# Optimization experiments

Hardware: AMD Instinct MI355X
Metric: run time of the kernel (lower is better)

Reference implementation:

```python
import jax, jax.numpy as jnp
import numpy as np

# Fixed supermask = [3, 4, 16, 28, 0, 0, 0, 3]:
#   preproc: relu(Linear x3); l1 = GCN(x); l2 = GCN(l1); l3 = GCN(l2);
#   out = relu(Linear z3((l1+l2+l3)/3))
HIDDEN = 64


def gcn_conv(h, W, b, src, dst, norm, n_nodes):
    # PyG GCNConv: h' = scatter_add(norm * (hW)[src] -> dst) + b
    hw = h @ W                                  # [N, F]
    msg = hw[src] * norm[:, None]               # gather + scale  [E+N, F]
    agg = jax.ops.segment_sum(msg, dst, num_segments=n_nodes)
    return agg + b


def setup_inputs() -> dict:
    key = jax.random.key(0)
    ks = jax.random.split(key, 12)
    N, E, NFEAT, NCLASS = 100000, 1000000, 256, 40
    x = jax.random.normal(ks[0], (N, NFEAT), dtype=jnp.float32)
    edge_index = jax.random.randint(ks[1], (2, E), 0, N, dtype=jnp.int64)
    s = 1.0 / np.sqrt(NFEAT)
    h = 1.0 / np.sqrt(HIDDEN)
    return {
        "x": x,
        "edge_index": edge_index,
        "Wx": jax.random.uniform(ks[2], (NFEAT, HIDDEN), jnp.float32, -s, s),
        "bx": jnp.zeros((HIDDEN,), jnp.float32),
        "W1": jax.random.uniform(ks[3], (HIDDEN, HIDDEN), jnp.float32, -h, h),
        "b1": jnp.zeros((HIDDEN,), jnp.float32),
        "W2": jax.random.uniform(ks[4], (HIDDEN, HIDDEN), jnp.float32, -h, h),
        "b2": jnp.zeros((HIDDEN,), jnp.float32),
        "W3": jax.random.uniform(ks[5], (HIDDEN, HIDDEN), jnp.float32, -h, h),
        "b3": jnp.zeros((HIDDEN,), jnp.float32),
        "Wz": jax.random.uniform(ks[6], (HIDDEN, NCLASS), jnp.float32, -h, h),
        "bz": jnp.zeros((NCLASS,), jnp.float32),
    }


def reference(x, edge_index, Wx, bx, W1, b1, W2, b2, W3, b3, Wz, bz):
    n = x.shape[0]
    # add self-loops (PyG GCNConv default)
    loop = jnp.arange(n, dtype=edge_index.dtype)
    src = jnp.concatenate([edge_index[0], loop])
    dst = jnp.concatenate([edge_index[1], loop])
    deg = jax.ops.segment_sum(jnp.ones_like(dst, dtype=x.dtype), dst, num_segments=n)
    dinv = jnp.where(deg > 0, jax.lax.rsqrt(deg), 0.0)
    norm = dinv[src] * dinv[dst]                 # [E+N]

    h0 = jax.nn.relu(x @ Wx + bx)                # x_3(relu) o x3(Linear)
    l1 = gcn_conv(h0, W1, b1, src, dst, norm, n)
    l2 = gcn_conv(l1, W2, b2, src, dst, norm, n)
    l3 = gcn_conv(l2, W3, b3, src, dst, norm, n)
    z = (l1 + l2 + l3) / 3.0
    return jax.nn.relu(z @ Wz + bz)
```

## Files before the change

### kernel.cpp

```cpp
#include <hip/hip_runtime.h>

#define NFEAT 256
#define HID 64
#define NCLASS 40
#define EPB 2048
#define BCAP 8192

typedef _Float16 half8 __attribute__((ext_vector_type(8)));
typedef float floatx4 __attribute__((ext_vector_type(4)));

__device__ __forceinline__ int wave_iscan(int v, int lane) {
    #pragma unroll
    for (int o = 1; o < 64; o <<= 1) {
        int u = __shfl_up(v, o, 64);
        if (lane >= o) v += u;
    }
    return v;
}

template<int NT>
__device__ __forceinline__ int block_iscan(int v, int t, int* wsum) {
    const int NW = NT / 64;
    int lane = t & 63, wv = t >> 6;
    int s = wave_iscan(v, lane);
    if (lane == 63) wsum[wv] = s;
    __syncthreads();
    if (wv == 0) {
        int w = (lane < NW) ? wsum[lane] : 0;
        #pragma unroll
        for (int o = 1; o < NW; o <<= 1) {
            int u = __shfl_up(w, o, 64);
            if (lane >= o) w += u;
        }
        if (lane < NW) wsum[lane] = w;
    }
    __syncthreads();
    int add = (wv > 0) ? wsum[wv - 1] : 0;
    return s + add;
}

struct BinSM {
    int lcnt[256], loff[256], lcur[256], gbase[256], wsum[4];
    int sdst[EPB];
    int words[EPB];
};
#define WT_BYTES (64 * 264 * 2)
#define SMSZ (sizeof(BinSM) > WT_BYTES ? sizeof(BinSM) : WT_BYTES)

__global__ __launch_bounds__(256) void k_pre(const int* __restrict__ src, const int* __restrict__ dst,
                                             int* __restrict__ bcur, int* __restrict__ bwords,
                                             int nbuckets, int E, int nbin,
                                             const float* __restrict__ W1, const float* __restrict__ W2,
                                             const float* __restrict__ W3, _Float16* __restrict__ Wt16,
                                             const float* __restrict__ x, const float* __restrict__ Wx,
                                             const float* __restrict__ bx, _Float16* __restrict__ h0,
                                             int N, int ngemm) {
    __shared__ __align__(16) char smraw[SMSZ];
    int t = threadIdx.x;
    int bid = blockIdx.x;

    if (bid >= nbin && bid < nbin + 3) {
        int l = bid - nbin;
        const float* Ws = (l == 0) ? W1 : (l == 1) ? W2 : W3;
        _Float16* wt = Wt16 + l * 4096;
        for (int i = t; i < 4096; i += 256) {
            int col = i >> 6, k = i & 63;
            wt[i] = (_Float16)Ws[k * HID + col];
        }
        return;
    }

    if (bid >= nbin + 3) {
        _Float16 (*Wt)[264] = (_Float16 (*)[264])smraw;
        {
            int c = t & 63, k0 = (t >> 6) * 64;
            for (int k = k0; k < k0 + 64; ++k)
                Wt[c][k] = (_Float16)Wx[k * HID + c];
        }
        __syncthreads();
        int lane = t & 63, wv = t >> 6;
        int lg = lane >> 4, ln = lane & 15;
        int gb = bid - nbin - 3;
        int wid = gb * 4 + wv;
        int nw = ngemm * 4;
        float bb[4];
        #pragma unroll
        for (int g = 0; g < 4; ++g) bb[g] = bx[g * 16 + ln];
        int ntiles = N >> 4;
        for (int tile = wid; tile < ntiles; tile += nw) {
            int row0 = tile << 4;
            const float* xr = x + (size_t)(row0 + ln) * NFEAT + lg * 8;
            float4 av[16];
            #pragma unroll
            for (int ks = 0; ks < 8; ++ks) {
                av[2 * ks]     = *(const float4*)(xr + ks * 32);
                av[2 * ks + 1] = *(const float4*)(xr + ks * 32 + 4);
            }
            floatx4 acc[4] = {{0.f,0.f,0.f,0.f},{0.f,0.f,0.f,0.f},{0.f,0.f,0.f,0.f},{0.f,0.f,0.f,0.f}};
            #pragma unroll
            for (int ks = 0; ks < 8; ++ks) {
                float4 a0 = av[2 * ks], a1 = av[2 * ks + 1];
                half8 a;
                a[0]=(_Float16)a0.x; a[1]=(_Float16)a0.y; a[2]=(_Float16)a0.z; a[3]=(_Float16)a0.w;
                a[4]=(_Float16)a1.x; a[5]=(_Float16)a1.y; a[6]=(_Float16)a1.z; a[7]=(_Float16)a1.w;
                #pragma unroll
                for (int g = 0; g < 4; ++g) {
                    half8 b = *(const half8*)&Wt[g * 16 + ln][ks * 32 + lg * 8];
                    acc[g] = __builtin_amdgcn_mfma_f32_16x16x32_f16(a, b, acc[g], 0, 0, 0);
                }
            }
            #pragma unroll
            for (int g = 0; g < 4; ++g) {
                #pragma unroll
                for (int r = 0; r < 4; ++r) {
                    int row = row0 + lg * 4 + r;
                    h0[(size_t)row * HID + g * 16 + ln] = (_Float16)fmaxf(acc[g][r] + bb[g], 0.f);
                }
            }
        }
        return;
    }

    BinSM* sm = (BinSM*)smraw;
    int base = bid * EPB;
    int n = E - base; if (n > EPB) n = EPB;
    sm->lcnt[t] = 0;
    __syncthreads();
    for (int i = t; i < n; i += 256) {
        int d = dst[base + i];
        sm->sdst[i] = d;
        atomicAdd(&sm->lcnt[d >> 9], 1);
    }
    __syncthreads();
    int v = sm->lcnt[t];
    int incl = block_iscan<256>(v, t, sm->wsum);
    int excl = incl - v;
    sm->loff[t] = excl; sm->lcur[t] = excl;
    __syncthreads();
    for (int i = t; i < n; i += 256) {
        int d = sm->sdst[i], s = src[base + i];
        int b = d >> 9;
        int p = atomicAdd(&sm->lcur[b], 1);
        sm->words[p] = s | ((d & 511) << 17);
    }
    __syncthreads();
    if (t < nbuckets) {
        int c = sm->lcnt[t];
        sm->gbase[t] = c > 0 ? atomicAdd(&bcur[t], c) : 0;
    }
    __syncthreads();
    int lane = t & 63, wv = t >> 6;
    for (int b = wv; b < nbuckets; b += 4) {
        int o = sm->loff[b], c = sm->lcnt[b], gb = sm->gbase[b];
        int* dstp = bwords + (size_t)b * BCAP;
        for (int i = lane; i < c; i += 64) {
            int gp = gb + i;
            if (gp < BCAP) dstp[gp] = sm->words[o + i];
        }
    }
}

__global__ __launch_bounds__(256) void k_csr(const int* __restrict__ bcur, const int* __restrict__ bwords,
                                             int* __restrict__ csr, unsigned* __restrict__ pk,
                                             float* __restrict__ dinv, int N) {
    __shared__ int cnt[512], cur[512], wsum[4];
    __shared__ int lcsr[BCAP];
    int t = threadIdx.x;
    int b = blockIdx.x;
    int nodebase = b << 9;
    int nb = bcur[b]; if (nb > BCAP) nb = BCAP;
    cnt[t] = 0; cnt[t + 256] = 0;
    __syncthreads();
    const int* wp = bwords + (size_t)b * BCAP;
    for (int i = t; i < nb; i += 256)
        atomicAdd(&cnt[wp[i] >> 17], 1);
    __syncthreads();
    int v0 = cnt[2 * t], v1 = cnt[2 * t + 1];
    int p = v0 + v1;
    int incl = block_iscan<256>(p, t, wsum);
    int e = incl - p;
    cur[2 * t] = e; cur[2 * t + 1] = e + v0;
    #pragma unroll
    for (int j = 0; j < 2; ++j) {
        int node = nodebase + 2 * t + j;
        if (node < N) {
            int c = cnt[2 * t + j]; if (c > 2047) c = 2047;
            pk[node] = (unsigned)(b * BCAP + cur[2 * t + j]) | ((unsigned)c << 21);
            dinv[node] = rsqrtf((float)c + 1.0f);
        }
    }
    __syncthreads();
    for (int i = t; i < nb; i += 256) {
        int w = wp[i];
        int pos = atomicAdd(&cur[w >> 17], 1);
        lcsr[pos] = w & 0x1FFFF;
    }
    __syncthreads();
    int* cp = csr + (size_t)b * BCAP;
    for (int i = t; i < nb; i += 256) cp[i] = lcsr[i];
}

template<int WRN>
__global__ __launch_bounds__(256) void k_layer(const _Float16* __restrict__ Ph, const int* __restrict__ csr,
                                               const unsigned* __restrict__ pk, const float* __restrict__ dinv,
                                               const _Float16* __restrict__ Wt, const float* __restrict__ b,
                                               float* __restrict__ normf,
                                               _Float16* __restrict__ Lout, int N) {
    __shared__ _Float16 z[32][72];
    __shared__ _Float16 ot[32][72];
    int t = threadIdx.x;
    int lane = t & 63, wv = t >> 6;
    int sg = lane >> 3, f8 = lane & 7;
    int lg = lane >> 4, ln = lane & 15;
    int nb = blockIdx.x << 5;
    int node = nb + wv * 8 + sg;
    bool valid = node < N;
    int nodec = valid ? node : (N - 1);
    int col = wv * 16 + ln;
    half8 bf0 = *(const half8*)(Wt + col * 64 + lg * 8);
    half8 bf1 = *(const half8*)(Wt + col * 64 + 32 + lg * 8);
    float bb = b[col];

    unsigned pkv = valid ? pk[node] : 0u;
    int off = (int)(pkv & 0x1FFFFFu);
    int c = valid ? (int)(pkv >> 21) : 0;
    float dd = valid ? dinv[node] : 0.f;
    const _Float16* pb = Ph + f8 * 8;
    float acc[8];
    {
        half8 self = *(const half8*)(pb + (size_t)nodec * HID);
        float dd2 = dd * dd;
        #pragma unroll
        for (int j = 0; j < 8; ++j) acc[j] = (float)self[j] * dd2;
    }
    int ecur = f8;
    bool ok = ecur < c;
    int s_cur = ok ? csr[off + ecur] : nodec;
    float nm_cur;
    if (WRN) {
        nm_cur = ok ? dinv[s_cur] * dd : 0.f;
        if (ok) normf[off + ecur] = nm_cur;
    } else {
        nm_cur = ok ? normf[off + ecur] : 0.f;
    }
    for (int jj = 0; jj < c; jj += 8) {
        int en = jj + 8 + f8;
        bool okn = en < c;
        int s_nxt = okn ? csr[off + en] : nodec;
        float nm_nxt;
        if (WRN) {
            nm_nxt = okn ? dinv[s_nxt] * dd : 0.f;
            if (okn) normf[off + en] = nm_nxt;
        } else {
            nm_nxt = okn ? normf[off + en] : 0.f;
        }
        #pragma unroll
        for (int j = 0; j < 8; ++j) {
            int ss = __shfl(s_cur, j, 8);
            float nn = __shfl(nm_cur, j, 8);
            half8 v = *(const half8*)(pb + (size_t)ss * HID);
            #pragma unroll
            for (int q = 0; q < 8; ++q) acc[q] = fmaf((float)v[q], nn, acc[q]);
        }
        s_cur = s_nxt; nm_cur = nm_nxt;
    }
    {
        half8 zv;
        #pragma unroll
        for (int j = 0; j < 8; ++j) zv[j] = (_Float16)acc[j];
        *(half8*)&z[wv * 8 + sg][f8 * 8] = zv;
    }
    __syncthreads();
    floatx4 acc0 = {0.f, 0.f, 0.f, 0.f}, acc1 = {0.f, 0.f, 0.f, 0.f};
    {
        half8 a0 = *(const half8*)&z[ln][lg * 8];
        half8 a1 = *(const half8*)&z[16 + ln][lg * 8];
        acc0 = __builtin_amdgcn_mfma_f32_16x16x32_f16(a0, bf0, acc0, 0, 0, 0);
        acc1 = __builtin_amdgcn_mfma_f32_16x16x32_f16(a1, bf0, acc1, 0, 0, 0);
        a0 = *(const half8*)&z[ln][32 + lg * 8];
        a1 = *(const half8*)&z[16 + ln][32 + lg * 8];
        acc0 = __builtin_amdgcn_mfma_f32_16x16x32_f16(a0, bf1, acc0, 0, 0, 0);
        acc1 = __builtin_amdgcn_mfma_f32_16x16x32_f16(a1, bf1, acc1, 0, 0, 0);
    }
    #pragma unroll
    for (int r = 0; r < 4; ++r) {
        ot[lg * 4 + r][wv * 16 + ln] = (_Float16)(acc0[r] + bb);
        ot[16 + lg * 4 + r][wv * 16 + ln] = (_Float16)(acc1[r] + bb);
    }
    __syncthreads();
    {
        int row = t >> 3, c8 = t & 7;
        int onode = nb + row;
        if (onode < N)
            *(half8*)(Lout + (size_t)onode * HID + c8 * 8) = *(const half8*)&ot[row][c8 * 8];
    }
}

__global__ __launch_bounds__(256) void k_gemm_out(const _Float16* __restrict__ L1, const _Float16* __restrict__ L2,
                                                  const _Float16* __restrict__ L3, const float* __restrict__ Wz,
                                                  const float* __restrict__ bz, float* __restrict__ outp, int N) {
    int t = threadIdx.x;
    int lane = t & 63, lg = lane >> 4, ln = lane & 15;
    int wid = (blockIdx.x * 256 + t) >> 6;
    int nw = (gridDim.x * 256) >> 6;
    half8 b[2][3];
    float bb[3];
    #pragma unroll
    for (int g = 0; g < 3; ++g) {
        int col = g * 16 + ln;
        bb[g] = (col < NCLASS) ? bz[col] : 0.f;
        #pragma unroll
        for (int ks = 0; ks < 2; ++ks)
            #pragma unroll
            for (int j = 0; j < 8; ++j)
                b[ks][g][j] = (col < NCLASS) ? (_Float16)(Wz[(ks * 32 + lg * 8 + j) * NCLASS + col] * (1.f / 3.f)) : (_Float16)0.f;
    }
    int ntiles = N >> 4;
    for (int tile = wid; tile < ntiles; tile += nw) {
        int row0 = tile << 4;
        size_t rb = (size_t)(row0 + ln) * HID + lg * 8;
        floatx4 acc[3] = {{0.f,0.f,0.f,0.f},{0.f,0.f,0.f,0.f},{0.f,0.f,0.f,0.f}};
        #pragma unroll
        for (int ks = 0; ks < 2; ++ks) {
            half8 a1 = *(const half8*)(L1 + rb + ks * 32);
            half8 a2 = *(const half8*)(L2 + rb + ks * 32);
            half8 a3 = *(const half8*)(L3 + rb + ks * 32);
            half8 a;
            #pragma unroll
            for (int j = 0; j < 8; ++j)
                a[j] = (_Float16)((float)a1[j] + (float)a2[j] + (float)a3[j]);
            #pragma unroll
            for (int g = 0; g < 3; ++g)
                acc[g] = __builtin_amdgcn_mfma_f32_16x16x32_f16(a, b[ks][g], acc[g], 0, 0, 0);
        }
        #pragma unroll
        for (int g = 0; g < 3; ++g) {
            int col = g * 16 + ln;
            if (col < NCLASS) {
                #pragma unroll
                for (int r = 0; r < 4; ++r)
                    outp[(size_t)(row0 + lg * 4 + r) * NCLASS + col] = fmaxf(acc[g][r] + bb[g], 0.f);
            }
        }
    }
}

extern "C" void kernel_launch(void* const* d_in, const int* in_sizes, int n_in,
                              void* d_out, int out_size, void* d_ws, size_t ws_size,
                              hipStream_t stream) {
    const float* x  = (const float*)d_in[0];
    const int*   ei = (const int*)d_in[1];
    const float* Wx = (const float*)d_in[2];
    const float* bx = (const float*)d_in[3];
    const float* W1 = (const float*)d_in[4];
    const float* b1 = (const float*)d_in[5];
    const float* W2 = (const float*)d_in[6];
    const float* b2 = (const float*)d_in[7];
    const float* W3 = (const float*)d_in[8];
    const float* b3 = (const float*)d_in[9];
    const float* Wz = (const float*)d_in[10];
    const float* bz = (const float*)d_in[11];
    float* out = (float*)d_out;

    int N = in_sizes[0] / NFEAT;
    int E = in_sizes[1] / 2;
    const int* src = ei;
    const int* dst = ei + E;
    int nbuckets = (N + 511) >> 9;

    size_t nh = (size_t)N * HID;
    size_t Npad = ((size_t)N + 7) / 8 * 8;
    int*      bcur = (int*)d_ws;
    float*    dinv = (float*)d_ws + 256;
    unsigned* pk   = (unsigned*)(dinv + Npad);
    _Float16* H0   = (_Float16*)(pk + Npad);
    _Float16* L1   = H0 + nh;
    _Float16* L2   = L1 + nh;
    _Float16* L3   = L2 + nh;
    int*      bwords = (int*)(L3 + nh);
    int*      csr  = bwords + (size_t)nbuckets * BCAP;
    _Float16* Wt16 = (_Float16*)(csr + (size_t)nbuckets * BCAP);
    float*    normf = (float*)(Wt16 + 3 * 4096);

    int nbin = (E + EPB - 1) / EPB;
    int ngemm = 512;
    hipMemsetAsync(bcur, 0, 256 * sizeof(int), stream);
    k_pre<<<nbin + 3 + ngemm, 256, 0, stream>>>(src, dst, bcur, bwords, nbuckets, E, nbin,
                                                W1, W2, W3, Wt16, x, Wx, bx, H0, N, ngemm);
    k_csr<<<nbuckets, 256, 0, stream>>>(bcur, bwords, csr, pk, dinv, N);

    int layer_blocks = (N + 31) / 32;
    k_layer<1><<<layer_blocks, 256, 0, stream>>>(H0, csr, pk, dinv, Wt16,          b1, normf, L1, N);
    k_layer<0><<<layer_blocks, 256, 0, stream>>>(L1, csr, pk, dinv, Wt16 + 4096,   b2, normf, L2, N);
    k_layer<0><<<layer_blocks, 256, 0, stream>>>(L2, csr, pk, dinv, Wt16 + 8192,   b3, normf, L3, N);

    k_gemm_out<<<512, 256, 0, stream>>>(L1, L2, L3, Wz, bz, out, N);
}
```

Measured before the change: 292.9 us.

## Split input GEMM across binning and CSR kernels to overlap with graph build

The dense x@Wx GEMM tiles are divided into two halves. One half runs in extra blocks of the edge-binning kernel and the other in extra blocks of the CSR-building kernel, so each graph preprocessing stage overlaps with part of the GEMM. The edges-per-block count for binning is doubled, which halves the number of binning blocks. The CSR kernel's shared memory becomes a union sized to fit the GEMM weight tile, and the larger EPB raises per-block shared memory in k_pre, which may reduce occupancy.

```diff
diff --git a/kernel.cpp b/kernel.cpp
--- a/kernel.cpp
+++ b/kernel.cpp
@@ -3,7 +3,7 @@
 #define NFEAT 256
 #define HID 64
 #define NCLASS 40
-#define EPB 2048
+#define EPB 4096
 #define BCAP 8192
 
 typedef _Float16 half8 __attribute__((ext_vector_type(8)));
@@ -39,13 +39,62 @@
     return s + add;
 }
 
+__device__ __forceinline__ void gemm_tiles(char* smraw, int t, int wid, int nw,
+                                           const float* __restrict__ x, const float* __restrict__ Wx,
+                                           const float* __restrict__ bx, _Float16* __restrict__ h0,
+                                           int tile0, int tile1) {
+    _Float16 (*Wt)[264] = (_Float16 (*)[264])smraw;
+    {
+        int c = t & 63, k0 = (t >> 6) * 64;
+        for (int k = k0; k < k0 + 64; ++k)
+            Wt[c][k] = (_Float16)Wx[k * HID + c];
+    }
+    __syncthreads();
+    int lane = t & 63;
+    int lg = lane >> 4, ln = lane & 15;
+    float bb[4];
+    #pragma unroll
+    for (int g = 0; g < 4; ++g) bb[g] = bx[g * 16 + ln];
+    for (int tile = tile0 + wid; tile < tile1; tile += nw) {
+        int row0 = tile << 4;
+        const float* xr = x + (size_t)(row0 + ln) * NFEAT + lg * 8;
+        float4 av[16];
+        #pragma unroll
+        for (int ks = 0; ks < 8; ++ks) {
+            av[2 * ks]     = *(const float4*)(xr + ks * 32);
+            av[2 * ks + 1] = *(const float4*)(xr + ks * 32 + 4);
+        }
+        floatx4 acc[4] = {{0.f,0.f,0.f,0.f},{0.f,0.f,0.f,0.f},{0.f,0.f,0.f,0.f},{0.f,0.f,0.f,0.f}};
+        #pragma unroll
+        for (int ks = 0; ks < 8; ++ks) {
+            float4 a0 = av[2 * ks], a1 = av[2 * ks + 1];
+            half8 a;
+            a[0]=(_Float16)a0.x; a[1]=(_Float16)a0.y; a[2]=(_Float16)a0.z; a[3]=(_Float16)a0.w;
+            a[4]=(_Float16)a1.x; a[5]=(_Float16)a1.y; a[6]=(_Float16)a1.z; a[7]=(_Float16)a1.w;
+            #pragma unroll
+            for (int g = 0; g < 4; ++g) {
+                half8 b = *(const half8*)&Wt[g * 16 + ln][ks * 32 + lg * 8];
+                acc[g] = __builtin_amdgcn_mfma_f32_16x16x32_f16(a, b, acc[g], 0, 0, 0);
+            }
+        }
+        #pragma unroll
+        for (int g = 0; g < 4; ++g) {
+            #pragma unroll
+            for (int r = 0; r < 4; ++r) {
+                int row = row0 + lg * 4 + r;
+                h0[(size_t)row * HID + g * 16 + ln] = (_Float16)fmaxf(acc[g][r] + bb[g], 0.f);
+            }
+        }
+    }
+}
+
 struct BinSM {
     int lcnt[256], loff[256], lcur[256], gbase[256], wsum[4];
     int sdst[EPB];
     int words[EPB];
 };
 #define WT_BYTES (64 * 264 * 2)
-#define SMSZ (sizeof(BinSM) > WT_BYTES ? sizeof(BinSM) : WT_BYTES)
+#define SMSZ1 (sizeof(BinSM) > (size_t)WT_BYTES ? sizeof(BinSM) : (size_t)WT_BYTES)
 
 __global__ __launch_bounds__(256) void k_pre(const int* __restrict__ src, const int* __restrict__ dst,
                                              int* __restrict__ bcur, int* __restrict__ bwords,
@@ -54,8 +103,8 @@
                                              const float* __restrict__ W3, _Float16* __restrict__ Wt16,
                                              const float* __restrict__ x, const float* __restrict__ Wx,
                                              const float* __restrict__ bx, _Float16* __restrict__ h0,
-                                             int N, int ngemm) {
-    __shared__ __align__(16) char smraw[SMSZ];
+                                             int N, int ngemm, int tile0, int tile1) {
+    __shared__ __align__(16) char smraw[SMSZ1];
     int t = threadIdx.x;
     int bid = blockIdx.x;
 
@@ -71,53 +120,9 @@
     }
 
     if (bid >= nbin + 3) {
-        _Float16 (*Wt)[264] = (_Float16 (*)[264])smraw;
-        {
-            int c = t & 63, k0 = (t >> 6) * 64;
-            for (int k = k0; k < k0 + 64; ++k)
-                Wt[c][k] = (_Float16)Wx[k * HID + c];
-        }
-        __syncthreads();
-        int lane = t & 63, wv = t >> 6;
-        int lg = lane >> 4, ln = lane & 15;
-        int gb = bid - nbin - 3;
-        int wid = gb * 4 + wv;
-        int nw = ngemm * 4;
-        float bb[4];
-        #pragma unroll
-        for (int g = 0; g < 4; ++g) bb[g] = bx[g * 16 + ln];
-        int ntiles = N >> 4;
-        for (int tile = wid; tile < ntiles; tile += nw) {
-            int row0 = tile << 4;
-            const float* xr = x + (size_t)(row0 + ln) * NFEAT + lg * 8;
-            float4 av[16];
-            #pragma unroll
-            for (int ks = 0; ks < 8; ++ks) {
-                av[2 * ks]     = *(const float4*)(xr + ks * 32);
-                av[2 * ks + 1] = *(const float4*)(xr + ks * 32 + 4);
-            }
-            floatx4 acc[4] = {{0.f,0.f,0.f,0.f},{0.f,0.f,0.f,0.f},{0.f,0.f,0.f,0.f},{0.f,0.f,0.f,0.f}};
-            #pragma unroll
-            for (int ks = 0; ks < 8; ++ks) {
-                float4 a0 = av[2 * ks], a1 = av[2 * ks + 1];
-                half8 a;
-                a[0]=(_Float16)a0.x; a[1]=(_Float16)a0.y; a[2]=(_Float16)a0.z; a[3]=(_Float16)a0.w;
-                a[4]=(_Float16)a1.x; a[5]=(_Float16)a1.y; a[6]=(_Float16)a1.z; a[7]=(_Float16)a1.w;
-                #pragma unroll
-                for (int g = 0; g < 4; ++g) {
-                    half8 b = *(const half8*)&Wt[g * 16 + ln][ks * 32 + lg * 8];
-                    acc[g] = __builtin_amdgcn_mfma_f32_16x16x32_f16(a, b, acc[g], 0, 0, 0);
-                }
-            }
-            #pragma unroll
-            for (int g = 0; g < 4; ++g) {
-                #pragma unroll
-                for (int r = 0; r < 4; ++r) {
-                    int row = row0 + lg * 4 + r;
-                    h0[(size_t)row * HID + g * 16 + ln] = (_Float16)fmaxf(acc[g][r] + bb[g], 0.f);
-                }
-            }
-        }
+        int wv = t >> 6;
+        int wid = (bid - nbin - 3) * 4 + wv;
+        gemm_tiles(smraw, t, wid, ngemm * 4, x, Wx, bx, h0, tile0, tile1);
         return;
     }
 
@@ -160,44 +165,62 @@
     }
 }
 
+struct CsrSM {
+    int cnt[512], cur[512], wsum[4];
+    int lcsr[BCAP];
+};
+#define SMSZ2 (sizeof(CsrSM) > (size_t)WT_BYTES ? sizeof(CsrSM) : (size_t)WT_BYTES)
+
 __global__ __launch_bounds__(256) void k_csr(const int* __restrict__ bcur, const int* __restrict__ bwords,
                                              int* __restrict__ csr, unsigned* __restrict__ pk,
-                                             float* __restrict__ dinv, int N) {
-    __shared__ int cnt[512], cur[512], wsum[4];
-    __shared__ int lcsr[BCAP];
+                                             float* __restrict__ dinv, int N, int ncsr,
+                                             const float* __restrict__ x, const float* __restrict__ Wx,
+                                             const float* __restrict__ bx, _Float16* __restrict__ h0,
+                                             int ngemm, int tile0, int tile1) {
+    __shared__ __align__(16) char smraw[SMSZ2];
     int t = threadIdx.x;
-    int b = blockIdx.x;
+    int bid = blockIdx.x;
+
+    if (bid >= ncsr) {
+        int wv = t >> 6;
+        int wid = (bid - ncsr) * 4 + wv;
+        gemm_tiles(smraw, t, wid, ngemm * 4, x, Wx, bx, h0, tile0, tile1);
+        return;
+    }
+
+    CsrSM* sm = (CsrSM*)smraw;
+    int b = bid;
     int nodebase = b << 9;
     int nb = bcur[b]; if (nb > BCAP) nb = BCAP;
-    cnt[t] = 0; cnt[t + 256] = 0;
+    sm->cnt[t] = 0; sm->cnt[t + 256] = 0;
     __syncthreads();
     const int* wp = bwords + (size_t)b * BCAP;
     for (int i = t; i < nb; i += 256)
-        atomicAdd(&cnt[wp[i] >> 17], 1);
-    __syncthreads();
-    int v0 = cnt[2 * t], v1 = cnt[2 * t + 1];
+        atomicAdd(&sm->cnt[wp[i] >> 17], 1);
+    __syncthreads();
+    int v0 = sm->cnt[2 * t], v1 = sm->cnt[2 * t + 1];
     int p = v0 + v1;
-    int incl = block_iscan<256>(p, t, wsum);
+    int incl = block_iscan<256>(p, t, sm->wsum);
     int e = incl - p;
-    cur[2 * t] = e; cur[2 * t + 1] = e + v0;
+    sm->cur[2 * t] = e; sm->cur[2 * t + 1] = e + v0;
     #pragma unroll
     for (int j = 0; j < 2; ++j) {
         int node = nodebase + 2 * t + j;
         if (node < N) {
-            int c = cnt[2 * t + j]; if (c > 2047) c = 2047;
-            pk[node] = (unsigned)(b * BCAP + cur[2 * t + j]) | ((unsigned)c << 21);
+            int c = sm->cnt[2 * t + j]; if (c > 2047) c = 2047;
+            pk[node] = (unsigned)(b * BCAP + sm->cur[2 * t + j]) | ((unsigned)c << 21);
             dinv[node] = rsqrtf((float)c + 1.0f);
         }
     }
     __syncthreads();
     for (int i = t; i < nb; i += 256) {
         int w = wp[i];
-        int pos = atomicAdd(&cur[w >> 17], 1);
-        lcsr[pos] = w & 0x1FFFF;
+        int pos = atomicAdd(&sm->cur[w >> 17], 1);
+        sm->lcsr[pos] = w & 0x1FFFF;
     }
     __syncthreads();
     int* cp = csr + (size_t)b * BCAP;
-    for (int i = t; i < nb; i += 256) cp[i] = lcsr[i];
+    for (int i = t; i < nb; i += 256) cp[i] = sm->lcsr[i];
 }
 
 template<int WRN>
@@ -383,11 +406,15 @@
     float*    normf = (float*)(Wt16 + 3 * 4096);
 
     int nbin = (E + EPB - 1) / EPB;
-    int ngemm = 512;
+    int ngemm1 = 256, ngemm2 = 256;
+    int ntiles = N >> 4;
+    int half = (ntiles / 2) & ~3;
     hipMemsetAsync(bcur, 0, 256 * sizeof(int), stream);
-    k_pre<<<nbin + 3 + ngemm, 256, 0, stream>>>(src, dst, bcur, bwords, nbuckets, E, nbin,
-                                                W1, W2, W3, Wt16, x, Wx, bx, H0, N, ngemm);
-    k_csr<<<nbuckets, 256, 0, stream>>>(bcur, bwords, csr, pk, dinv, N);
+    k_pre<<<nbin + 3 + ngemm1, 256, 0, stream>>>(src, dst, bcur, bwords, nbuckets, E, nbin,
+                                                 W1, W2, W3, Wt16, x, Wx, bx, H0, N,
+                                                 ngemm1, 0, half);
+    k_csr<<<nbuckets + ngemm2, 256, 0, stream>>>(bcur, bwords, csr, pk, dinv, N, nbuckets,
+                                                 x, Wx, bx, H0, ngemm2, half, ntiles);
 
     int layer_blocks = (N + 31) / 32;
     k_layer<1><<<layer_blocks, 256, 0, stream>>>(H0, csr, pk, dinv, Wt16,          b1, normf, L1, N);
```

Result: no change. 297.7 us (+1.6%).
